# Optimization experiments

Hardware: AMD Instinct MI355X
Metric: run time of the kernel (lower is better)

The kernel has to match this reference:

```python
import jax, jax.numpy as jnp
import numpy as np

B, L, D = 256, 512, 768


def setup_inputs() -> dict:
    key = jax.random.key(0)
    k1, k2, k3, k4, k5, k6 = jax.random.split(key, 6)
    final_hidden = jax.random.normal(k1, (B, L, D), dtype=jnp.float32)
    attention_mask = jax.random.randint(k2, (B, L), 0, 2, dtype=jnp.int32)
    W13 = jax.random.normal(k3, (13, 4, D), dtype=jnp.float32) * 0.02
    b13 = jax.random.normal(k4, (13, 4), dtype=jnp.float32) * 0.02
    W14 = jax.random.normal(k5, (2, D), dtype=jnp.float32) * 0.02
    b14 = jax.random.normal(k6, (2,), dtype=jnp.float32) * 0.02
    return {"final_hidden": final_hidden, "attention_mask": attention_mask,
            "W13": W13, "b13": b13, "W14": W14, "b14": b14}


def reference(final_hidden, attention_mask, W13, b13, W14, b14):
    # Fused masked mean pooling: zero out padded positions, sum over seq,
    # divide by per-row valid-token count (replaces the per-element loops).
    mask = attention_mask.astype(final_hidden.dtype)            # [B, L]
    pooled = jnp.einsum('bl,bld->bd', mask, final_hidden)       # [B, D]
    pooled = pooled / mask.sum(axis=1, keepdims=True)           # [B, D]
    # 13 heads of out-dim 4 (batched as one einsum) + one head of out-dim 2.
    out13 = jnp.einsum('bd,kod->bko', pooled, W13) + b13        # [B, 13, 4]
    out14 = pooled @ W14.T + b14                                # [B, 2]
    # Original returns a list of 14 tensors; we concat along the last dim
    # ([B, 13*4 + 2] = [B, 54]) which preserves all values.
    return jnp.concatenate([out13.reshape(out13.shape[0], -1), out14], axis=-1)
```

## Files before the change

### kernel.cpp

```cpp
#include <hip/hip_runtime.h>

#define BATCH 256
#define SEQ   512
#define DIM   768
#define D4    (DIM / 4)
#define NOUT  54

__global__ __launch_bounds__(256) void pool_partial_kernel(
    const float* __restrict__ fh, const int* __restrict__ mask,
    float* __restrict__ partial, int S, int Ls)
{
    const int b    = blockIdx.x / S;
    const int s    = blockIdx.x - b * S;
    const int tid  = threadIdx.x;
    const int lane = tid & 63;
    const int grp  = tid >> 6;

    __shared__ int list[128];
    __shared__ unsigned long long balls[2];

    const int base_l = s * Ls;
    const int nw     = Ls >> 6;

    int my_m = 0, my_l = 0;
    unsigned long long my_ball = 0;
    if (grp < nw) {
        my_l = base_l + tid;
        my_m = mask[b * SEQ + my_l];
        my_ball = __ballot(my_m != 0);
        if (lane == 0) balls[grp] = my_ball;
    }
    __syncthreads();

    int n = __popcll(balls[0]);
    if (nw > 1) n += __popcll(balls[1]);

    if (grp < nw && my_m != 0) {
        int off = (grp == 1) ? __popcll(balls[0]) : 0;
        int pre = off + __popcll(my_ball & ((1ull << lane) - 1));
        list[pre] = my_l;
    }
    __syncthreads();

    const float4* fh4 = (const float4*)fh + (size_t)b * SEQ * D4;

    float4 a0 = make_float4(0.f, 0.f, 0.f, 0.f);
    float4 a1 = a0, a2 = a0;

    int i = grp;
    for (; i + 4 < n; i += 8) {
        const float4* r0 = fh4 + (size_t)list[i]     * D4;
        const float4* r1 = fh4 + (size_t)list[i + 4] * D4;
        float4 x0 = r0[lane], x1 = r0[lane + 64], x2 = r0[lane + 128];
        float4 y0 = r1[lane], y1 = r1[lane + 64], y2 = r1[lane + 128];
        a0.x += x0.x + y0.x; a0.y += x0.y + y0.y;
        a0.z += x0.z + y0.z; a0.w += x0.w + y0.w;
        a1.x += x1.x + y1.x; a1.y += x1.y + y1.y;
        a1.z += x1.z + y1.z; a1.w += x1.w + y1.w;
        a2.x += x2.x + y2.x; a2.y += x2.y + y2.y;
        a2.z += x2.z + y2.z; a2.w += x2.w + y2.w;
    }
    if (i < n) {
        const float4* r0 = fh4 + (size_t)list[i] * D4;
        float4 x0 = r0[lane], x1 = r0[lane + 64], x2 = r0[lane + 128];
        a0.x += x0.x; a0.y += x0.y; a0.z += x0.z; a0.w += x0.w;
        a1.x += x1.x; a1.y += x1.y; a1.z += x1.z; a1.w += x1.w;
        a2.x += x2.x; a2.y += x2.y; a2.z += x2.z; a2.w += x2.w;
    }

    __shared__ float4 red[4][D4];
    red[grp][lane]       = a0;
    red[grp][lane + 64]  = a1;
    red[grp][lane + 128] = a2;
    __syncthreads();

    if (tid < D4) {
        float4 r0 = red[0][tid], r1 = red[1][tid], r2 = red[2][tid], r3 = red[3][tid];
        float4 sum = make_float4(r0.x + r1.x + r2.x + r3.x,
                                 r0.y + r1.y + r2.y + r3.y,
                                 r0.z + r1.z + r2.z + r3.z,
                                 r0.w + r1.w + r2.w + r3.w);
        ((float4*)partial)[((size_t)b * S + s) * D4 + tid] = sum;
    }
}

__global__ __launch_bounds__(256) void finalize_kernel(
    const float* __restrict__ partial, const int* __restrict__ mask,
    const float* __restrict__ W13, const float* __restrict__ b13,
    const float* __restrict__ W14, const float* __restrict__ b14,
    float* __restrict__ out, int S)
{
    const int b    = blockIdx.x;
    const int tid  = threadIdx.x;
    const int lane = tid & 63;
    const int wave = tid >> 6;

    int cnt = mask[b * SEQ + tid] + mask[b * SEQ + 256 + tid];
    for (int off = 32; off; off >>= 1) cnt += __shfl_down(cnt, off);
    __shared__ int wcnt[4];
    if (lane == 0) wcnt[wave] = cnt;

    __shared__ float pooled[DIM];
    __syncthreads();
    const float inv = 1.0f / (float)(wcnt[0] + wcnt[1] + wcnt[2] + wcnt[3]);

    if (tid < D4) {
        float4 acc = make_float4(0.f, 0.f, 0.f, 0.f);
        const float4* p4 = (const float4*)partial + (size_t)b * S * D4 + tid;
        for (int s = 0; s < S; ++s) {
            float4 v = p4[(size_t)s * D4];
            acc.x += v.x; acc.y += v.y; acc.z += v.z; acc.w += v.w;
        }
        ((float4*)pooled)[tid] =
            make_float4(acc.x * inv, acc.y * inv, acc.z * inv, acc.w * inv);
    }
    __syncthreads();

    for (int o = wave; o < NOUT; o += 4) {
        const float* Wrow = (o < 52) ? (W13 + (size_t)o * DIM)
                                     : (W14 + (size_t)(o - 52) * DIM);
        const float bias  = (o < 52) ? b13[o] : b14[o - 52];
        float acc = 0.f;
        #pragma unroll
        for (int j = 0; j < 12; ++j) {
            const int d = lane + 64 * j;
            acc = fmaf(pooled[d], Wrow[d], acc);
        }
        for (int off = 32; off; off >>= 1) acc += __shfl_down(acc, off);
        if (lane == 0) out[(size_t)b * NOUT + o] = acc + bias;
    }
}

extern "C" void kernel_launch(void* const* d_in, const int* in_sizes, int n_in,
                              void* d_out, int out_size, void* d_ws, size_t ws_size,
                              hipStream_t stream) {
    const float* fh   = (const float*)d_in[0];
    const int*   mask = (const int*)d_in[1];
    const float* W13  = (const float*)d_in[2];
    const float* b13  = (const float*)d_in[3];
    const float* W14  = (const float*)d_in[4];
    const float* b14  = (const float*)d_in[5];
    float*       out  = (float*)d_out;
    float*       partial = (float*)d_ws;

    int S = 8;
    while (S > 4 && (size_t)BATCH * S * DIM * sizeof(float) > ws_size) S >>= 1;
    const int Ls = SEQ / S;

    pool_partial_kernel<<<dim3(BATCH * S), dim3(256), 0, stream>>>(
        fh, mask, partial, S, Ls);
    finalize_kernel<<<dim3(BATCH), dim3(256), 0, stream>>>(
        partial, mask, W13, b13, W14, b14, out, S);
}
```

Measured before the change: 499.1 us.

## Fuse masked pooling and head projection into one 1024-thread-per-row kernel

Replaces the two-kernel pipeline (per-segment partial sums written to workspace, then a finalize kernel) with a single kernel that assigns one 1024-thread block to each batch row. The block compacts the whole mask into a shared index list, gathers valid rows across 16 waves, reduces them in shared memory and applies the 54-output projection directly. This removes the workspace round-trip, the second launch and the recount of the mask. In exchange there are fewer blocks (one per row), fewer resident waves per CU and a larger shared-memory footprint, which may reduce memory-level parallelism.

Measured after the change: 486.9 us. 2.5% less time.

```diff
diff --git a/kernel.cpp b/kernel.cpp
--- a/kernel.cpp
+++ b/kernel.cpp
@@ -6,39 +6,38 @@
 #define D4    (DIM / 4)
 #define NOUT  54
 
-__global__ __launch_bounds__(256) void pool_partial_kernel(
+__global__ __launch_bounds__(1024) void bow_fused_kernel(
     const float* __restrict__ fh, const int* __restrict__ mask,
-    float* __restrict__ partial, int S, int Ls)
+    const float* __restrict__ W13, const float* __restrict__ b13,
+    const float* __restrict__ W14, const float* __restrict__ b14,
+    float* __restrict__ out)
 {
-    const int b    = blockIdx.x / S;
-    const int s    = blockIdx.x - b * S;
+    const int b    = blockIdx.x;
     const int tid  = threadIdx.x;
     const int lane = tid & 63;
-    const int grp  = tid >> 6;
+    const int wave = tid >> 6;
 
-    __shared__ int list[128];
-    __shared__ unsigned long long balls[2];
+    __shared__ unsigned long long balls[8];
+    __shared__ int   list[SEQ];
+    __shared__ float pooled[DIM];
 
-    const int base_l = s * Ls;
-    const int nw     = Ls >> 6;
-
-    int my_m = 0, my_l = 0;
-    unsigned long long my_ball = 0;
-    if (grp < nw) {
-        my_l = base_l + tid;
-        my_m = mask[b * SEQ + my_l];
-        my_ball = __ballot(my_m != 0);
-        if (lane == 0) balls[grp] = my_ball;
+    int my_m = 0;
+    if (wave < 8) {
+        my_m = mask[b * SEQ + tid];
+        unsigned long long bl = __ballot(my_m != 0);
+        if (lane == 0) balls[wave] = bl;
     }
     __syncthreads();
 
-    int n = __popcll(balls[0]);
-    if (nw > 1) n += __popcll(balls[1]);
+    int n = 0;
+    #pragma unroll
+    for (int w = 0; w < 8; ++w) n += __popcll(balls[w]);
 
-    if (grp < nw && my_m != 0) {
-        int off = (grp == 1) ? __popcll(balls[0]) : 0;
-        int pre = off + __popcll(my_ball & ((1ull << lane) - 1));
-        list[pre] = my_l;
+    if (wave < 8 && my_m != 0) {
+        int off = 0;
+        for (int w = 0; w < wave; ++w) off += __popcll(balls[w]);
+        const unsigned long long bl = balls[wave];
+        list[off + __popcll(bl & ((1ull << lane) - 1))] = tid;
     }
     __syncthreads();
 
@@ -47,10 +46,10 @@
     float4 a0 = make_float4(0.f, 0.f, 0.f, 0.f);
     float4 a1 = a0, a2 = a0;
 
-    int i = grp;
-    for (; i + 4 < n; i += 8) {
-        const float4* r0 = fh4 + (size_t)list[i]     * D4;
-        const float4* r1 = fh4 + (size_t)list[i + 4] * D4;
+    int i = wave;
+    for (; i + 16 < n; i += 32) {
+        const float4* r0 = fh4 + (size_t)list[i]      * D4;
+        const float4* r1 = fh4 + (size_t)list[i + 16] * D4;
         float4 x0 = r0[lane], x1 = r0[lane + 64], x2 = r0[lane + 128];
         float4 y0 = r1[lane], y1 = r1[lane + 64], y2 = r1[lane + 128];
         a0.x += x0.x + y0.x; a0.y += x0.y + y0.y;
@@ -68,47 +67,18 @@
         a2.x += x2.x; a2.y += x2.y; a2.z += x2.z; a2.w += x2.w;
     }
 
-    __shared__ float4 red[4][D4];
-    red[grp][lane]       = a0;
-    red[grp][lane + 64]  = a1;
-    red[grp][lane + 128] = a2;
+    __shared__ float4 red[16][D4];
+    red[wave][lane]       = a0;
+    red[wave][lane + 64]  = a1;
+    red[wave][lane + 128] = a2;
     __syncthreads();
 
-    if (tid < D4) {
-        float4 r0 = red[0][tid], r1 = red[1][tid], r2 = red[2][tid], r3 = red[3][tid];
-        float4 sum = make_float4(r0.x + r1.x + r2.x + r3.x,
-                                 r0.y + r1.y + r2.y + r3.y,
-                                 r0.z + r1.z + r2.z + r3.z,
-                                 r0.w + r1.w + r2.w + r3.w);
-        ((float4*)partial)[((size_t)b * S + s) * D4 + tid] = sum;
-    }
-}
-
-__global__ __launch_bounds__(256) void finalize_kernel(
-    const float* __restrict__ partial, const int* __restrict__ mask,
-    const float* __restrict__ W13, const float* __restrict__ b13,
-    const float* __restrict__ W14, const float* __restrict__ b14,
-    float* __restrict__ out, int S)
-{
-    const int b    = blockIdx.x;
-    const int tid  = threadIdx.x;
-    const int lane = tid & 63;
-    const int wave = tid >> 6;
-
-    int cnt = mask[b * SEQ + tid] + mask[b * SEQ + 256 + tid];
-    for (int off = 32; off; off >>= 1) cnt += __shfl_down(cnt, off);
-    __shared__ int wcnt[4];
-    if (lane == 0) wcnt[wave] = cnt;
-
-    __shared__ float pooled[DIM];
-    __syncthreads();
-    const float inv = 1.0f / (float)(wcnt[0] + wcnt[1] + wcnt[2] + wcnt[3]);
-
+    const float inv = 1.0f / (float)n;
     if (tid < D4) {
         float4 acc = make_float4(0.f, 0.f, 0.f, 0.f);
-        const float4* p4 = (const float4*)partial + (size_t)b * S * D4 + tid;
-        for (int s = 0; s < S; ++s) {
-            float4 v = p4[(size_t)s * D4];
+        #pragma unroll
+        for (int w = 0; w < 16; ++w) {
+            float4 v = red[w][tid];
             acc.x += v.x; acc.y += v.y; acc.z += v.z; acc.w += v.w;
         }
         ((float4*)pooled)[tid] =
@@ -116,7 +86,7 @@
     }
     __syncthreads();
 
-    for (int o = wave; o < NOUT; o += 4) {
+    for (int o = wave; o < NOUT; o += 16) {
         const float* Wrow = (o < 52) ? (W13 + (size_t)o * DIM)
                                      : (W14 + (size_t)(o - 52) * DIM);
         const float bias  = (o < 52) ? b13[o] : b14[o - 52];
@@ -141,14 +111,7 @@
     const float* W14  = (const float*)d_in[4];
     const float* b14  = (const float*)d_in[5];
     float*       out  = (float*)d_out;
-    float*       partial = (float*)d_ws;
 
-    int S = 8;
-    while (S > 4 && (size_t)BATCH * S * DIM * sizeof(float) > ws_size) S >>= 1;
-    const int Ls = SEQ / S;
-
-    pool_partial_kernel<<<dim3(BATCH * S), dim3(256), 0, stream>>>(
-        fh, mask, partial, S, Ls);
-    finalize_kernel<<<dim3(BATCH), dim3(256), 0, stream>>>(
-        partial, mask, W13, b13, W14, b14, out, S);
+    bow_fused_kernel<<<dim3(BATCH), dim3(1024), 0, stream>>>(
+        fh, mask, W13, b13, W14, b14, out);
 }
```
